# Performance work log

Hardware: AMD Instinct MI355X
Metric: run time of the kernel (lower is better)

## Reference

```python
import jax, jax.numpy as jnp
import numpy as np

B, L, S, H, E = 2, 2048, 2048, 16, 64


def setup_inputs() -> dict:
    key = jax.random.key(0)
    kq, kk, kv = jax.random.split(key, 3)
    queries = jax.random.normal(kq, (B, L, H, E), dtype=jnp.float32)
    keys = jax.random.normal(kk, (B, S, H, E), dtype=jnp.float32)
    values = jax.random.normal(kv, (B, S, H, E), dtype=jnp.float32)
    attn_mask = jnp.ones((B, 1, L, S), dtype=jnp.float32)  # >0.5 means attend
    return {"queries": queries, "keys": keys, "values": values, "attn_mask": attn_mask}


def reference(queries, keys, values, attn_mask):
    # queries: [B,L,H,E], keys/values: [B,S,H,E], attn_mask broadcastable to [B,H,L,S]
    E_ = queries.shape[-1]
    scale = 1.0 / np.sqrt(E_).astype(np.float32)
    scores = jnp.einsum('blhe,bshe->bhls', queries, keys)  # [B,H,L,S]
    large_negative = jnp.float32(-1e9)
    scores = scores + jnp.where(attn_mask > 0.5, jnp.float32(0.0), large_negative)
    A = jax.nn.softmax(scale * scores, axis=-1)  # dropout p=0.0 -> identity
    V = jnp.einsum('bhls,bshd->bhld', A, values)  # [B,H,L,D]
    return V
```

## Files before the change

kernel.cpp:

```cpp
#include <hip/hip_runtime.h>

typedef float    f32x4 __attribute__((ext_vector_type(4)));
typedef _Float16 f16x2 __attribute__((ext_vector_type(2)));
typedef _Float16 f16x4 __attribute__((ext_vector_type(4)));
typedef _Float16 f16x8 __attribute__((ext_vector_type(8)));
typedef int      i32x4 __attribute__((ext_vector_type(4)));

namespace {
constexpr int B_ = 2, L_ = 2048, S_ = 2048, H_ = 16, E_ = 64;
constexpr int MBLK = 128;
constexpr int NT = 128;
constexpr int NTILES = S_ / NT;
constexpr int KPAD = 72;
constexpr int VPAD = 136;

#define SCALE2f 0.1803368801111204f
#define MBIAS2f -1.8033688e8f

__device__ __forceinline__ f16x2 cvt2(float a, float b) {
  return __builtin_bit_cast(f16x2, __builtin_amdgcn_cvt_pkrtz(a, b));
}
__device__ __forceinline__ int pkh(float a, float b) {
  return __builtin_bit_cast(int, __builtin_amdgcn_cvt_pkrtz(a, b));
}
union H8 { f16x8 v; i32x4 i; };
union H4 { f16x4 v; f16x2 h[2]; };
}

extern "C" __global__ __launch_bounds__(256)
void maskpack_kernel(const float* __restrict__ Mg, unsigned long long* __restrict__ Wb) {
  const int w    = (int)((blockIdx.x * 256 + threadIdx.x) >> 6);
  const int lane = threadIdx.x & 63;
  const float* src = Mg + (size_t)w * 2048 + lane;
  unsigned long long* dst = Wb + (size_t)w * 32;
#pragma unroll 8
  for (int j = 0; j < 32; ++j) {
    const unsigned long long bits = __ballot(src[j * 64] > 0.5f);
    if (lane == 0) dst[j] = bits;
  }
}

extern "C" __global__ __launch_bounds__(256, 2)
void fattn_kernel(const float* __restrict__ Qg, const float* __restrict__ Kg,
                  const float* __restrict__ Vg, const unsigned long long* __restrict__ Wb,
                  float* __restrict__ Og) {
  __shared__ __align__(16) _Float16 Ks[2][NT][KPAD];
  __shared__ __align__(16) _Float16 Vt[2][E_][VPAD];

  const int tid  = threadIdx.x;
  const int wv   = tid >> 6;
  const int lane = tid & 63;
  const int qd   = lane >> 4;
  const int cl   = lane & 15;

  const int bid = blockIdx.x;
  const int qb  = bid >> 5;
  const int bh  = bid & 31;
  const int h   = bh & (H_ - 1);
  const int b   = bh >> 4;

  const int l0 = qb * MBLK + wv * 32;

  f16x8 qf[2][2];
#pragma unroll
  for (int mt = 0; mt < 2; ++mt) {
    const float* qp = Qg + ((((size_t)b * L_ + (l0 + mt * 16 + cl)) * H_ + h) << 6);
#pragma unroll
    for (int kb = 0; kb < 2; ++kb) {
      const int e0 = qd * 8 + kb * 32;
      f32x4 x = *(const f32x4*)(qp + e0);
      f32x4 y = *(const f32x4*)(qp + e0 + 4);
      H8 u;
      u.i = (i32x4){pkh(x[0], x[1]), pkh(x[2], x[3]), pkh(y[0], y[1]), pkh(y[2], y[3])};
      qf[mt][kb] = u.v;
    }
  }

  const int krow = tid >> 2;
  const int kc0  = (tid & 3) << 4;
  const int vcol = tid & 31;
  const int ve0  = (tid >> 5) << 3;

  const float* kptr = Kg + ((((size_t)b * S_ + krow) * H_ + h) << 6) + kc0;
  const float* vptr = Vg + ((((size_t)b * S_ + 2 * vcol) * H_ + h) << 6) + ve0;
  const size_t rs64 = (size_t)64 * H_ * E_;
  const size_t rs1  = (size_t)H_ * E_;
  const size_t tstep = (size_t)NT * H_ * E_;

  const unsigned long long* wbp = Wb + (((size_t)b * L_ + (l0 + cl)) << 5);

  f32x4 kr[8], vA0[2], vA1[2], vB0[2], vB1[2];
  auto load_kv = [&](int t) {
    const float* kp = kptr + (size_t)t * tstep;
    const float* vp = vptr + (size_t)t * tstep;
#pragma unroll
    for (int i = 0; i < 4; ++i) {
      kr[i]     = *(const f32x4*)(kp + i * 4);
      kr[i + 4] = *(const f32x4*)(kp + rs64 + i * 4);
    }
    vA0[0] = *(const f32x4*)(vp + 0);               vA0[1] = *(const f32x4*)(vp + 4);
    vA1[0] = *(const f32x4*)(vp + rs1 + 0);         vA1[1] = *(const f32x4*)(vp + rs1 + 4);
    vB0[0] = *(const f32x4*)(vp + rs64 + 0);        vB0[1] = *(const f32x4*)(vp + rs64 + 4);
    vB1[0] = *(const f32x4*)(vp + rs64 + rs1 + 0);  vB1[1] = *(const f32x4*)(vp + rs64 + rs1 + 4);
  };
  auto stage_kv = [&](int buf) {
#pragma unroll
    for (int hh = 0; hh < 2; ++hh) {
      i32x4 w0 = {pkh(kr[4*hh+0][0], kr[4*hh+0][1]), pkh(kr[4*hh+0][2], kr[4*hh+0][3]),
                  pkh(kr[4*hh+1][0], kr[4*hh+1][1]), pkh(kr[4*hh+1][2], kr[4*hh+1][3])};
      i32x4 w1 = {pkh(kr[4*hh+2][0], kr[4*hh+2][1]), pkh(kr[4*hh+2][2], kr[4*hh+2][3]),
                  pkh(kr[4*hh+3][0], kr[4*hh+3][1]), pkh(kr[4*hh+3][2], kr[4*hh+3][3])};
      *(i32x4*)&Ks[buf][krow + 64*hh][kc0]     = w0;
      *(i32x4*)&Ks[buf][krow + 64*hh][kc0 + 8] = w1;
    }
#pragma unroll
    for (int j = 0; j < 8; ++j) {
      *(f16x2*)&Vt[buf][ve0 + j][2 * vcol]      = cvt2(vA0[j>>2][j&3], vA1[j>>2][j&3]);
      *(f16x2*)&Vt[buf][ve0 + j][2 * vcol + 64] = cvt2(vB0[j>>2][j&3], vB1[j>>2][j&3]);
    }
  };

  const f32x4 zero4 = {0.f, 0.f, 0.f, 0.f};
  f32x4 acc[2][4];
#pragma unroll
  for (int mt = 0; mt < 2; ++mt)
#pragma unroll
    for (int et = 0; et < 4; ++et) acc[mt][et] = zero4;
  f32x4 rs4[2] = {zero4, zero4};

  load_kv(0);
  stage_kv(0);
  load_kv(1);
  unsigned long long mw[2] = {wbp[0], wbp[1]};

  for (int t = 0; t < NTILES; ++t) {
    const int cb = t & 1;
    __syncthreads();

    unsigned long long mwn0 = 0, mwn1 = 0;
    if (t + 1 < NTILES) { mwn0 = wbp[2 * (t + 1)]; mwn1 = wbp[2 * (t + 1) + 1]; }

    if (t + 1 < NTILES) stage_kv(cb ^ 1);
    if (t + 2 < NTILES) load_kv(t + 2);

#pragma unroll
    for (int sub = 0; sub < 2; ++sub) {
      const int sb = sub * 64;
      f32x4 sc[4][2];
#pragma unroll
      for (int nt = 0; nt < 4; ++nt) {
        const f16x8 a0 = *(const f16x8*)&Ks[cb][sb + nt * 16 + cl][qd * 8];
        const f16x8 a1 = *(const f16x8*)&Ks[cb][sb + nt * 16 + cl][qd * 8 + 32];
#pragma unroll
        for (int mt = 0; mt < 2; ++mt) {
          f32x4 c = zero4;
          c = __builtin_amdgcn_mfma_f32_16x16x32_f16(a0, qf[mt][0], c, 0, 0, 0);
          c = __builtin_amdgcn_mfma_f32_16x16x32_f16(a1, qf[mt][1], c, 0, 0, 0);
          sc[nt][mt] = c;
        }
      }

      f16x4 pa[2][4];
      const unsigned long long w = mw[sub];
      if (w == ~0ull) {
#pragma unroll
        for (int mt = 0; mt < 2; ++mt)
#pragma unroll
          for (int nt = 0; nt < 4; ++nt) {
            f32x4 p;
#pragma unroll
            for (int r = 0; r < 4; ++r)
              p[r] = __builtin_amdgcn_exp2f(sc[nt][mt][r] * SCALE2f);
            rs4[mt] += p;
            H4 u;
            u.h[0] = cvt2(p[0], p[1]);
            u.h[1] = cvt2(p[2], p[3]);
            pa[mt][nt] = u.v;
          }
      } else {
        const unsigned lo = (unsigned)w;
        const unsigned hi = (unsigned)(w >> 32);
#pragma unroll
        for (int mt = 0; mt < 2; ++mt)
#pragma unroll
          for (int nt = 0; nt < 4; ++nt) {
            const unsigned sh = ((nt < 2) ? lo : hi) >> ((nt & 1) * 16 + qd * 4);
            f32x4 p;
#pragma unroll
            for (int r = 0; r < 4; ++r) {
              const float bias = (sh & (1u << r)) ? 0.f : MBIAS2f;
              p[r] = __builtin_amdgcn_exp2f(__builtin_fmaf(sc[nt][mt][r], SCALE2f, bias));
            }
            rs4[mt] += p;
            H4 u;
            u.h[0] = cvt2(p[0], p[1]);
            u.h[1] = cvt2(p[2], p[3]);
            pa[mt][nt] = u.v;
          }
      }

#pragma unroll
      for (int nt = 0; nt < 4; ++nt)
#pragma unroll
        for (int et = 0; et < 4; ++et) {
          const f16x4 bv = *(const f16x4*)&Vt[cb][et * 16 + cl][sb + nt * 16 + qd * 4];
          acc[0][et] = __builtin_amdgcn_mfma_f32_16x16x16f16(pa[0][nt], bv, acc[0][et], 0, 0, 0);
          acc[1][et] = __builtin_amdgcn_mfma_f32_16x16x16f16(pa[1][nt], bv, acc[1][et], 0, 0, 0);
        }
    }

    mw[0] = mwn0;
    mw[1] = mwn1;
  }

#pragma unroll
  for (int mt = 0; mt < 2; ++mt) {
    float v = rs4[mt][0] + rs4[mt][1] + rs4[mt][2] + rs4[mt][3];
    v += __shfl_xor(v, 16, 64);
    v += __shfl_xor(v, 32, 64);
#pragma unroll
    for (int r = 0; r < 4; ++r) {
      const float invq = 1.0f / __shfl(v, qd * 4 + r, 64);
      const int l = l0 + mt * 16 + qd * 4 + r;
      float* op = Og + ((((size_t)b * H_ + h) * L_ + l) << 6) + cl;
#pragma unroll
      for (int et = 0; et < 4; ++et) op[et * 16] = acc[mt][et][r] * invq;
    }
  }
}

extern "C" void kernel_launch(void* const* d_in, const int* in_sizes, int n_in,
                              void* d_out, int out_size, void* d_ws, size_t ws_size,
                              hipStream_t stream) {
  const float* Q = (const float*)d_in[0];
  const float* K = (const float*)d_in[1];
  const float* V = (const float*)d_in[2];
  const float* M = (const float*)d_in[3];
  float* O = (float*)d_out;
  unsigned long long* Wb = (unsigned long long*)d_ws;

  hipLaunchKernelGGL(maskpack_kernel, dim3(B_ * L_ / 4), dim3(256), 0, stream, M, Wb);
  hipLaunchKernelGGL(fattn_kernel, dim3(B_ * H_ * (L_ / MBLK)), dim3(256), 0, stream,
                     Q, K, V, Wb, O);
}
```

Measured before the change: 179.3 us.

## Preconvert K/V to fp16 head-major layouts and stream tiles via global_load_lds

```diff
diff --git a/kernel.cpp b/kernel.cpp
--- a/kernel.cpp
+++ b/kernel.cpp
@@ -9,14 +9,15 @@
 namespace {
 constexpr int B_ = 2, L_ = 2048, S_ = 2048, H_ = 16, E_ = 64;
 constexpr int MBLK = 128;
-constexpr int NT = 128;
+constexpr int NT = 64;
 constexpr int NTILES = S_ / NT;
-constexpr int KPAD = 72;
-constexpr int VPAD = 136;
 
 #define SCALE2f 0.1803368801111204f
 #define MBIAS2f -1.8033688e8f
 
+constexpr size_t KHOFF = (size_t)1 << 20;
+constexpr size_t VHOFF = KHOFF + (size_t)B_ * H_ * S_ * E_ * 2;
+
 __device__ __forceinline__ f16x2 cvt2(float a, float b) {
   return __builtin_bit_cast(f16x2, __builtin_amdgcn_cvt_pkrtz(a, b));
 }
@@ -25,6 +26,11 @@
 }
 union H8 { f16x8 v; i32x4 i; };
 union H4 { f16x4 v; f16x2 h[2]; };
+
+#define GLOAD_LDS16(g, l)                                              \
+  __builtin_amdgcn_global_load_lds(                                    \
+      (const __attribute__((address_space(1))) void*)(g),              \
+      (__attribute__((address_space(3))) void*)(l), 16, 0, 0)
 }
 
 extern "C" __global__ __launch_bounds__(256)
@@ -40,18 +46,57 @@
   }
 }
 
+extern "C" __global__ __launch_bounds__(256)
+void kcvt_kernel(const float* __restrict__ Kg, _Float16* __restrict__ Kh) {
+  const int idx = blockIdx.x * 256 + threadIdx.x;
+  const int j = idx & 7;
+  const int h = (idx >> 3) & (H_ - 1);
+  const int s = (idx >> 7) & (S_ - 1);
+  const int b = idx >> 18;
+  const float* src = Kg + ((((size_t)b * S_ + s) * H_ + h) << 6) + j * 8;
+  f32x4 x = *(const f32x4*)src, y = *(const f32x4*)(src + 4);
+  i32x4 w = {pkh(x[0], x[1]), pkh(x[2], x[3]), pkh(y[0], y[1]), pkh(y[2], y[3])};
+  *(i32x4*)(Kh + ((((size_t)b * H_ + h) * S_ + s) << 6) + j * 8) = w;
+}
+
+extern "C" __global__ __launch_bounds__(256)
+void vcvt_kernel(const float* __restrict__ Vg, _Float16* __restrict__ Vh) {
+  __shared__ _Float16 T[64][72];
+  const int bid = blockIdx.x;
+  const int st = bid & 31;
+  const int h  = (bid >> 5) & (H_ - 1);
+  const int b  = bid >> 9;
+  const int t  = threadIdx.x;
+  const int sl = t >> 2;
+  const int e0 = (t & 3) << 4;
+  const float* src = Vg + ((((size_t)b * S_ + st * 64 + sl) * H_ + h) << 6) + e0;
+#pragma unroll
+  for (int i = 0; i < 4; ++i) {
+    f32x4 x = *(const f32x4*)(src + i * 4);
+#pragma unroll
+    for (int c = 0; c < 4; ++c) T[e0 + i * 4 + c][sl] = (_Float16)x[c];
+  }
+  __syncthreads();
+  const int er = t >> 2;
+  const int s0 = (t & 3) << 4;
+  _Float16* dst = Vh + (((((size_t)b * H_ + h) << 6) + er) * S_) + st * 64 + s0;
+  *(i32x4*)dst       = *(const i32x4*)&T[er][s0];
+  *(i32x4*)(dst + 8) = *(const i32x4*)&T[er][s0 + 8];
+}
+
 extern "C" __global__ __launch_bounds__(256, 2)
-void fattn_kernel(const float* __restrict__ Qg, const float* __restrict__ Kg,
-                  const float* __restrict__ Vg, const unsigned long long* __restrict__ Wb,
+void fattn_kernel(const float* __restrict__ Qg, const _Float16* __restrict__ Kh,
+                  const _Float16* __restrict__ Vh, const unsigned long long* __restrict__ Wb,
                   float* __restrict__ Og) {
-  __shared__ __align__(16) _Float16 Ks[2][NT][KPAD];
-  __shared__ __align__(16) _Float16 Vt[2][E_][VPAD];
+  __shared__ __align__(16) _Float16 Ks[2][NT][64];
+  __shared__ __align__(16) _Float16 Vt[2][E_][64];
 
   const int tid  = threadIdx.x;
   const int wv   = tid >> 6;
   const int lane = tid & 63;
   const int qd   = lane >> 4;
   const int cl   = lane & 15;
+  const int sw   = cl & 7;
 
   const int bid = blockIdx.x;
   const int qb  = bid >> 5;
@@ -76,47 +121,22 @@
     }
   }
 
-  const int krow = tid >> 2;
-  const int kc0  = (tid & 3) << 4;
-  const int vcol = tid & 31;
-  const int ve0  = (tid >> 5) << 3;
-
-  const float* kptr = Kg + ((((size_t)b * S_ + krow) * H_ + h) << 6) + kc0;
-  const float* vptr = Vg + ((((size_t)b * S_ + 2 * vcol) * H_ + h) << 6) + ve0;
-  const size_t rs64 = (size_t)64 * H_ * E_;
-  const size_t rs1  = (size_t)H_ * E_;
-  const size_t tstep = (size_t)NT * H_ * E_;
+  const int rl  = lane >> 3;
+  const int gsl = lane & 7;
+  const int gsw = gsl ^ rl;
+  const _Float16* khb = Kh + ((((size_t)b * H_ + h) * S_) << 6);
+  const _Float16* vhb = Vh + ((((size_t)b * H_ + h) << 6) * (size_t)S_);
 
   const unsigned long long* wbp = Wb + (((size_t)b * L_ + (l0 + cl)) << 5);
 
-  f32x4 kr[8], vA0[2], vA1[2], vB0[2], vB1[2];
-  auto load_kv = [&](int t) {
-    const float* kp = kptr + (size_t)t * tstep;
-    const float* vp = vptr + (size_t)t * tstep;
-#pragma unroll
-    for (int i = 0; i < 4; ++i) {
-      kr[i]     = *(const f32x4*)(kp + i * 4);
-      kr[i + 4] = *(const f32x4*)(kp + rs64 + i * 4);
-    }
-    vA0[0] = *(const f32x4*)(vp + 0);               vA0[1] = *(const f32x4*)(vp + 4);
-    vA1[0] = *(const f32x4*)(vp + rs1 + 0);         vA1[1] = *(const f32x4*)(vp + rs1 + 4);
-    vB0[0] = *(const f32x4*)(vp + rs64 + 0);        vB0[1] = *(const f32x4*)(vp + rs64 + 4);
-    vB1[0] = *(const f32x4*)(vp + rs64 + rs1 + 0);  vB1[1] = *(const f32x4*)(vp + rs64 + rs1 + 4);
-  };
-  auto stage_kv = [&](int buf) {
-#pragma unroll
-    for (int hh = 0; hh < 2; ++hh) {
-      i32x4 w0 = {pkh(kr[4*hh+0][0], kr[4*hh+0][1]), pkh(kr[4*hh+0][2], kr[4*hh+0][3]),
-                  pkh(kr[4*hh+1][0], kr[4*hh+1][1]), pkh(kr[4*hh+1][2], kr[4*hh+1][3])};
-      i32x4 w1 = {pkh(kr[4*hh+2][0], kr[4*hh+2][1]), pkh(kr[4*hh+2][2], kr[4*hh+2][3]),
-                  pkh(kr[4*hh+3][0], kr[4*hh+3][1]), pkh(kr[4*hh+3][2], kr[4*hh+3][3])};
-      *(i32x4*)&Ks[buf][krow + 64*hh][kc0]     = w0;
-      *(i32x4*)&Ks[buf][krow + 64*hh][kc0 + 8] = w1;
-    }
-#pragma unroll
-    for (int j = 0; j < 8; ++j) {
-      *(f16x2*)&Vt[buf][ve0 + j][2 * vcol]      = cvt2(vA0[j>>2][j&3], vA1[j>>2][j&3]);
-      *(f16x2*)&Vt[buf][ve0 + j][2 * vcol + 64] = cvt2(vB0[j>>2][j&3], vB1[j>>2][j&3]);
+  auto dma = [&](int buf, int t) {
+#pragma unroll
+    for (int p = 0; p < 2; ++p) {
+      const int r0 = p * 32 + wv * 8;
+      const _Float16* ksrc = khb + (((size_t)(t * 64 + r0 + rl)) << 6) + gsw * 8;
+      GLOAD_LDS16(ksrc, &Ks[buf][r0][0]);
+      const _Float16* vsrc = vhb + (size_t)(r0 + rl) * S_ + t * 64 + gsw * 8;
+      GLOAD_LDS16(vsrc, &Vt[buf][r0][0]);
     }
   };
 
@@ -128,89 +148,81 @@
     for (int et = 0; et < 4; ++et) acc[mt][et] = zero4;
   f32x4 rs4[2] = {zero4, zero4};
 
-  load_kv(0);
-  stage_kv(0);
-  load_kv(1);
-  unsigned long long mw[2] = {wbp[0], wbp[1]};
+  dma(0, 0);
+  unsigned long long mwcur = wbp[0];
 
   for (int t = 0; t < NTILES; ++t) {
     const int cb = t & 1;
     __syncthreads();
 
-    unsigned long long mwn0 = 0, mwn1 = 0;
-    if (t + 1 < NTILES) { mwn0 = wbp[2 * (t + 1)]; mwn1 = wbp[2 * (t + 1) + 1]; }
-
-    if (t + 1 < NTILES) stage_kv(cb ^ 1);
-    if (t + 2 < NTILES) load_kv(t + 2);
-
-#pragma unroll
-    for (int sub = 0; sub < 2; ++sub) {
-      const int sb = sub * 64;
-      f32x4 sc[4][2];
-#pragma unroll
-      for (int nt = 0; nt < 4; ++nt) {
-        const f16x8 a0 = *(const f16x8*)&Ks[cb][sb + nt * 16 + cl][qd * 8];
-        const f16x8 a1 = *(const f16x8*)&Ks[cb][sb + nt * 16 + cl][qd * 8 + 32];
-#pragma unroll
-        for (int mt = 0; mt < 2; ++mt) {
-          f32x4 c = zero4;
-          c = __builtin_amdgcn_mfma_f32_16x16x32_f16(a0, qf[mt][0], c, 0, 0, 0);
-          c = __builtin_amdgcn_mfma_f32_16x16x32_f16(a1, qf[mt][1], c, 0, 0, 0);
-          sc[nt][mt] = c;
+    if (t + 1 < NTILES) dma(cb ^ 1, t + 1);
+    unsigned long long mwnext = 0;
+    if (t + 1 < NTILES) mwnext = wbp[t + 1];
+
+    f32x4 sc[4][2];
+#pragma unroll
+    for (int nt = 0; nt < 4; ++nt) {
+      const _Float16* krow = &Ks[cb][nt * 16 + cl][0];
+      const f16x8 a0 = *(const f16x8*)(krow + ((qd ^ sw) << 3));
+      const f16x8 a1 = *(const f16x8*)(krow + (((qd + 4) ^ sw) << 3));
+#pragma unroll
+      for (int mt = 0; mt < 2; ++mt) {
+        f32x4 c = zero4;
+        c = __builtin_amdgcn_mfma_f32_16x16x32_f16(a0, qf[mt][0], c, 0, 0, 0);
+        c = __builtin_amdgcn_mfma_f32_16x16x32_f16(a1, qf[mt][1], c, 0, 0, 0);
+        sc[nt][mt] = c;
+      }
+    }
+
+    f16x4 pa[2][4];
+    if (mwcur == ~0ull) {
+#pragma unroll
+      for (int mt = 0; mt < 2; ++mt)
+#pragma unroll
+        for (int nt = 0; nt < 4; ++nt) {
+          f32x4 p;
+#pragma unroll
+          for (int r = 0; r < 4; ++r)
+            p[r] = __builtin_amdgcn_exp2f(sc[nt][mt][r] * SCALE2f);
+          rs4[mt] += p;
+          H4 u;
+          u.h[0] = cvt2(p[0], p[1]);
+          u.h[1] = cvt2(p[2], p[3]);
+          pa[mt][nt] = u.v;
         }
+    } else {
+      const unsigned lo = (unsigned)mwcur;
+      const unsigned hi = (unsigned)(mwcur >> 32);
+#pragma unroll
+      for (int mt = 0; mt < 2; ++mt)
+#pragma unroll
+        for (int nt = 0; nt < 4; ++nt) {
+          const unsigned shm = ((nt < 2) ? lo : hi) >> ((nt & 1) * 16 + qd * 4);
+          f32x4 p;
+#pragma unroll
+          for (int r = 0; r < 4; ++r) {
+            const float bias = (shm & (1u << r)) ? 0.f : MBIAS2f;
+            p[r] = __builtin_amdgcn_exp2f(__builtin_fmaf(sc[nt][mt][r], SCALE2f, bias));
+          }
+          rs4[mt] += p;
+          H4 u;
+          u.h[0] = cvt2(p[0], p[1]);
+          u.h[1] = cvt2(p[2], p[3]);
+          pa[mt][nt] = u.v;
+        }
+    }
+
+#pragma unroll
+    for (int nt = 0; nt < 4; ++nt)
+#pragma unroll
+      for (int et = 0; et < 4; ++et) {
+        const _Float16* vrow = &Vt[cb][et * 16 + cl][0];
+        const f16x4 bv = *(const f16x4*)(vrow + ((((2 * nt + (qd >> 1)) ^ sw) << 3) + ((qd & 1) << 2)));
+        acc[0][et] = __builtin_amdgcn_mfma_f32_16x16x16f16(pa[0][nt], bv, acc[0][et], 0, 0, 0);
+        acc[1][et] = __builtin_amdgcn_mfma_f32_16x16x16f16(pa[1][nt], bv, acc[1][et], 0, 0, 0);
       }
 
-      f16x4 pa[2][4];
-      const unsigned long long w = mw[sub];
-      if (w == ~0ull) {
-#pragma unroll
-        for (int mt = 0; mt < 2; ++mt)
-#pragma unroll
-          for (int nt = 0; nt < 4; ++nt) {
-            f32x4 p;
-#pragma unroll
-            for (int r = 0; r < 4; ++r)
-              p[r] = __builtin_amdgcn_exp2f(sc[nt][mt][r] * SCALE2f);
-            rs4[mt] += p;
-            H4 u;
-            u.h[0] = cvt2(p[0], p[1]);
-            u.h[1] = cvt2(p[2], p[3]);
-            pa[mt][nt] = u.v;
-          }
-      } else {
-        const unsigned lo = (unsigned)w;
-        const unsigned hi = (unsigned)(w >> 32);
-#pragma unroll
-        for (int mt = 0; mt < 2; ++mt)
-#pragma unroll
-          for (int nt = 0; nt < 4; ++nt) {
-            const unsigned sh = ((nt < 2) ? lo : hi) >> ((nt & 1) * 16 + qd * 4);
-            f32x4 p;
-#pragma unroll
-            for (int r = 0; r < 4; ++r) {
-              const float bias = (sh & (1u << r)) ? 0.f : MBIAS2f;
-              p[r] = __builtin_amdgcn_exp2f(__builtin_fmaf(sc[nt][mt][r], SCALE2f, bias));
-            }
-            rs4[mt] += p;
-            H4 u;
-            u.h[0] = cvt2(p[0], p[1]);
-            u.h[1] = cvt2(p[2], p[3]);
-            pa[mt][nt] = u.v;
-          }
-      }
-
-#pragma unroll
-      for (int nt = 0; nt < 4; ++nt)
-#pragma unroll
-        for (int et = 0; et < 4; ++et) {
-          const f16x4 bv = *(const f16x4*)&Vt[cb][et * 16 + cl][sb + nt * 16 + qd * 4];
-          acc[0][et] = __builtin_amdgcn_mfma_f32_16x16x16f16(pa[0][nt], bv, acc[0][et], 0, 0, 0);
-          acc[1][et] = __builtin_amdgcn_mfma_f32_16x16x16f16(pa[1][nt], bv, acc[1][et], 0, 0, 0);
-        }
-    }
-
-    mw[0] = mwn0;
-    mw[1] = mwn1;
+    mwcur = mwnext;
   }
 
 #pragma unroll
@@ -238,8 +250,12 @@
   const float* M = (const float*)d_in[3];
   float* O = (float*)d_out;
   unsigned long long* Wb = (unsigned long long*)d_ws;
+  _Float16* Khp = (_Float16*)((char*)d_ws + KHOFF);
+  _Float16* Vhp = (_Float16*)((char*)d_ws + VHOFF);
 
   hipLaunchKernelGGL(maskpack_kernel, dim3(B_ * L_ / 4), dim3(256), 0, stream, M, Wb);
+  hipLaunchKernelGGL(kcvt_kernel, dim3(B_ * S_ * H_ * 8 / 256), dim3(256), 0, stream, K, Khp);
+  hipLaunchKernelGGL(vcvt_kernel, dim3(B_ * H_ * (S_ / 64)), dim3(256), 0, stream, V, Vhp);
   hipLaunchKernelGGL(fattn_kernel, dim3(B_ * H_ * (L_ / MBLK)), dim3(256), 0, stream,
-                     Q, K, V, Wb, O);
-}
+                     Q, Khp, Vhp, Wb, O);
+}
```

Measured after the change: 175.8 us. No clear change (-1.9%).
